# Performance work log

Hardware: AMD Instinct MI355X
Metric: run time of the kernel (lower is better)

## Reference

```python
import jax, jax.numpy as jnp
import numpy as np
from jax import lax

N, CIN, COUT, K = 16, 3, 16, 3
D = H = W = 64

def setup_inputs() -> dict:
    key = jax.random.key(0)
    k1, k2, k3 = jax.random.split(key, 3)
    x = jax.random.normal(k1, (N, CIN, D, H, W), dtype=jnp.float32)
    # torch Conv3d default init scale ~ 1/sqrt(fan_in); plain normals are fine for a baseline
    fan_in = CIN * K * K * K
    weight = jax.random.normal(k2, (COUT, CIN, K, K, K), dtype=jnp.float32) / np.sqrt(fan_in)
    bias = jax.random.normal(k3, (COUT,), dtype=jnp.float32) * 0.01
    return {"x": x, "weight": weight, "bias": bias}

def reference(x, weight, bias):
    # Conv3d, stride 1, no padding (NCDHW / OIDHW)
    y = lax.conv_general_dilated(
        x, weight,
        window_strides=(1, 1, 1),
        padding="VALID",
        dimension_numbers=("NCDHW", "OIDHW", "NCDHW"),
    )
    y = y + bias[None, :, None, None, None]          # [N, C, D', H', W']
    m = jnp.min(y, axis=2)                            # min over D -> [N, C, H', W']
    return jax.nn.softmax(m, axis=1)                  # softmax over channels
```

## Files before the change

kernel.cpp:

```cpp
#include <hip/hip_runtime.h>
#include <math.h>


#define CH 8

__global__ __launch_bounds__(1024)
__attribute__((amdgpu_waves_per_eu(8)))
void conv3d_min_softmax(
    const float* __restrict__ x,
    const float* __restrict__ wgt,
    const float* __restrict__ bias,
    float* __restrict__ out)
{
    const int tid = threadIdx.x;
    const int wv  = __builtin_amdgcn_readfirstlane(tid >> 6);
    const int l   = tid & 63;
    const int r0  = l >> 4;
    const int cg  = l & 15;
    const int wc  = cg * 2;
    const int n   = blockIdx.z;
    const int h0  = blockIdx.y * 4;
    const int w0  = blockIdx.x * 32;

    __shared__ __align__(16) float sx[2][5184];
    __shared__ float sm[128 * 17];

    const float bv = bias[wv];

    int goff[2];
#pragma unroll
    for (int k = 0; k < 2; ++k) {
        int F = tid + 1024 * k;
        if (F > 1295) F = 1295;
        int ci  = F / 432;
        int rem = F - ci * 432;
        int dd  = rem / 54;
        int rr  = rem - dd * 54;
        int rw  = rr / 9;
        int g   = rr - rw * 9;
        int gh  = h0 + rw;  if (gh > 63) gh = 63;
        int gw  = w0 + g * 4; if (gw > 60) gw = 60;
        goff[k] = (((ci * 64 + dd) * 64 + gh) * 64 + gw) * 4;
    }
    const char* xb = (const char*)(x + (size_t)n * 3 * 64 * 64 * 64);

    float Aacc[10][2];
#pragma unroll
    for (int j = 0; j < 10; ++j) { Aacc[j][0] = 0.f; Aacc[j][1] = 0.f; }
    float mv[2] = {1e30f, 1e30f};

    {
        char* lb = (char*)&sx[0][0];
        __builtin_amdgcn_global_load_lds(
            (const void*)(xb + goff[0]), (void*)(lb + tid * 16), 16, 0, 0);
        if (tid < 272)
            __builtin_amdgcn_global_load_lds(
                (const void*)(xb + goff[1]),
                (void*)(lb + (1024 + tid) * 16), 16, 0, 0);
    }

    for (int c = 0; c < 64 / CH; ++c) {
        __syncthreads();

        if (c < 7) {
            const char* xc = xb + (size_t)(c + 1) * (CH * 64 * 64 * 4);
            char* lb = (char*)&sx[(c + 1) & 1][0];
            __builtin_amdgcn_global_load_lds(
                (const void*)(xc + goff[0]), (void*)(lb + tid * 16),
                16, 0, 0);
            if (tid < 272)
                __builtin_amdgcn_global_load_lds(
                    (const void*)(xc + goff[1]),
                    (void*)(lb + (1024 + tid) * 16), 16, 0, 0);
        }

        const float* S = sx[c & 1];

#pragma unroll 1
        for (int ci = 0; ci < 3; ++ci) {
            float wsc[27];
            {
                const float* wp_ = wgt + (wv * 3 + ci) * 27;
#pragma unroll
                for (int i = 0; i < 27; ++i) wsc[i] = wp_[i];
            }
            const float* Sci = S + ci * (CH * 6 * 36) + r0 * 36 + wc;
#pragma unroll
            for (int dd = 0; dd < CH; ++dd) {
#pragma unroll
                for (int kh = 0; kh < 3; ++kh) {
                    const float2 a = *(const float2*)&Sci[(dd * 6 + kh) * 36];
                    const float2 b =
                        *(const float2*)&Sci[(dd * 6 + kh) * 36 + 2];
                    const float row[4] = {a.x, a.y, b.x, b.y};
#pragma unroll
                    for (int kw = 0; kw < 3; ++kw) {
                        const float wk0 = wsc[0  + kh * 3 + kw];
                        const float wk1 = wsc[9  + kh * 3 + kw];
                        const float wk2 = wsc[18 + kh * 3 + kw];
#pragma unroll
                        for (int p = 0; p < 2; ++p) {
                            const float xv = row[kw + p];
                            Aacc[dd + 2][p] = fmaf(xv, wk0, Aacc[dd + 2][p]);
                            Aacc[dd + 1][p] = fmaf(xv, wk1, Aacc[dd + 1][p]);
                            Aacc[dd + 0][p] = fmaf(xv, wk2, Aacc[dd + 0][p]);
                        }
                    }
                }
            }
        }

        const bool full = (c > 0);
#pragma unroll
        for (int j = 0; j < 8; ++j) {
            if (j >= 2 || full) {
                mv[0] = fminf(mv[0], Aacc[j][0]);
                mv[1] = fminf(mv[1], Aacc[j][1]);
            }
        }
#pragma unroll
        for (int p = 0; p < 2; ++p) {
            Aacc[0][p] = Aacc[8][p];
            Aacc[1][p] = Aacc[9][p];
        }
#pragma unroll
        for (int j = 2; j < 10; ++j) { Aacc[j][0] = 0.f; Aacc[j][1] = 0.f; }
    }

    const int px0 = r0 * 32 + wc;
    sm[px0 * 17 + wv]       = mv[0] + bv;
    sm[(px0 + 1) * 17 + wv] = mv[1] + bv;
    __syncthreads();

    const int hp = h0 + r0;
#pragma unroll
    for (int pp = 0; pp < 2; ++pp) {
        const int px = px0 + pp;
        float mx = -1e30f;
#pragma unroll
        for (int j = 0; j < 16; ++j) mx = fmaxf(mx, sm[px * 17 + j]);
        float sum = 0.f;
#pragma unroll
        for (int j = 0; j < 16; ++j) sum += __expf(sm[px * 17 + j] - mx);
        const int wp = w0 + wc + pp;
        if (hp < 62 && wp < 62) {
            const float e = __expf(sm[px * 17 + wv] - mx);
            out[(((size_t)n * 16 + wv) * 62 + hp) * 62 + wp] = e / sum;
        }
    }
}

extern "C" void kernel_launch(void* const* d_in, const int* in_sizes, int n_in,
                              void* d_out, int out_size, void* d_ws, size_t ws_size,
                              hipStream_t stream) {
    const float* x    = (const float*)d_in[0];
    const float* wgt  = (const float*)d_in[1];
    const float* bias = (const float*)d_in[2];
    float* out        = (float*)d_out;
    dim3 grid(2, 16, 16);
    dim3 block(1024);
    hipLaunchKernelGGL(conv3d_min_softmax, grid, block, 0, stream,
                       x, wgt, bias, out);
}
```

Before: 219.6 us.

## Enlarge per-thread tile to 4 outputs and block tile to 8 rows

Each thread now computes 4 adjacent W outputs instead of 2, and each block covers 8 H rows instead of 4, so the grid shrinks to 256 blocks. This reuses each LDS row load across more FMAs and lowers the halo overhead relative to the tile, cutting LDS traffic and redundant global loads. It roughly doubles accumulator registers, and the waves_per_eu(8) hint is dropped to allow that. The risks are lower occupancy and fewer blocks than needed to fill all CUs.

```diff
diff --git a/kernel.cpp b/kernel.cpp
--- a/kernel.cpp
+++ b/kernel.cpp
@@ -5,7 +5,6 @@
 #define CH 8
 
 __global__ __launch_bounds__(1024)
-__attribute__((amdgpu_waves_per_eu(8)))
 void conv3d_min_softmax(
     const float* __restrict__ x,
     const float* __restrict__ wgt,
@@ -15,27 +14,27 @@
     const int tid = threadIdx.x;
     const int wv  = __builtin_amdgcn_readfirstlane(tid >> 6);
     const int l   = tid & 63;
-    const int r0  = l >> 4;
-    const int cg  = l & 15;
-    const int wc  = cg * 2;
+    const int r0  = l >> 3;
+    const int cg  = l & 7;
+    const int wc  = cg * 4;
     const int n   = blockIdx.z;
-    const int h0  = blockIdx.y * 4;
+    const int h0  = blockIdx.y * 8;
     const int w0  = blockIdx.x * 32;
 
-    __shared__ __align__(16) float sx[2][5184];
-    __shared__ float sm[128 * 17];
+    __shared__ __align__(16) float sx[2][8640];
+    __shared__ float sm[256 * 17];
 
     const float bv = bias[wv];
 
-    int goff[2];
+    int goff[3];
 #pragma unroll
-    for (int k = 0; k < 2; ++k) {
+    for (int k = 0; k < 3; ++k) {
         int F = tid + 1024 * k;
-        if (F > 1295) F = 1295;
-        int ci  = F / 432;
-        int rem = F - ci * 432;
-        int dd  = rem / 54;
-        int rr  = rem - dd * 54;
+        if (F > 2159) F = 2159;
+        int ci  = F / 720;
+        int rem = F - ci * 720;
+        int dd  = rem / 90;
+        int rr  = rem - dd * 90;
         int rw  = rr / 9;
         int g   = rr - rw * 9;
         int gh  = h0 + rw;  if (gh > 63) gh = 63;
@@ -44,19 +43,24 @@
     }
     const char* xb = (const char*)(x + (size_t)n * 3 * 64 * 64 * 64);
 
-    float Aacc[10][2];
+    float Aacc[10][4];
 #pragma unroll
-    for (int j = 0; j < 10; ++j) { Aacc[j][0] = 0.f; Aacc[j][1] = 0.f; }
-    float mv[2] = {1e30f, 1e30f};
+    for (int j = 0; j < 10; ++j)
+#pragma unroll
+        for (int p = 0; p < 4; ++p) Aacc[j][p] = 0.f;
+    float mv[4] = {1e30f, 1e30f, 1e30f, 1e30f};
 
     {
         char* lb = (char*)&sx[0][0];
         __builtin_amdgcn_global_load_lds(
             (const void*)(xb + goff[0]), (void*)(lb + tid * 16), 16, 0, 0);
-        if (tid < 272)
+        __builtin_amdgcn_global_load_lds(
+            (const void*)(xb + goff[1]),
+            (void*)(lb + (1024 + tid) * 16), 16, 0, 0);
+        if (tid < 112)
             __builtin_amdgcn_global_load_lds(
-                (const void*)(xb + goff[1]),
-                (void*)(lb + (1024 + tid) * 16), 16, 0, 0);
+                (const void*)(xb + goff[2]),
+                (void*)(lb + (2048 + tid) * 16), 16, 0, 0);
     }
 
     for (int c = 0; c < 64 / CH; ++c) {
@@ -68,10 +72,13 @@
             __builtin_amdgcn_global_load_lds(
                 (const void*)(xc + goff[0]), (void*)(lb + tid * 16),
                 16, 0, 0);
-            if (tid < 272)
+            __builtin_amdgcn_global_load_lds(
+                (const void*)(xc + goff[1]),
+                (void*)(lb + (1024 + tid) * 16), 16, 0, 0);
+            if (tid < 112)
                 __builtin_amdgcn_global_load_lds(
-                    (const void*)(xc + goff[1]),
-                    (void*)(lb + (1024 + tid) * 16), 16, 0, 0);
+                    (const void*)(xc + goff[2]),
+                    (void*)(lb + (2048 + tid) * 16), 16, 0, 0);
         }
 
         const float* S = sx[c & 1];
@@ -84,22 +91,22 @@
 #pragma unroll
                 for (int i = 0; i < 27; ++i) wsc[i] = wp_[i];
             }
-            const float* Sci = S + ci * (CH * 6 * 36) + r0 * 36 + wc;
+            const float* Sci = S + ci * (CH * 10 * 36) + r0 * 36 + wc;
 #pragma unroll
             for (int dd = 0; dd < CH; ++dd) {
 #pragma unroll
                 for (int kh = 0; kh < 3; ++kh) {
-                    const float2 a = *(const float2*)&Sci[(dd * 6 + kh) * 36];
+                    const float4 a = *(const float4*)&Sci[(dd * 10 + kh) * 36];
                     const float2 b =
-                        *(const float2*)&Sci[(dd * 6 + kh) * 36 + 2];
-                    const float row[4] = {a.x, a.y, b.x, b.y};
+                        *(const float2*)&Sci[(dd * 10 + kh) * 36 + 4];
+                    const float row[6] = {a.x, a.y, a.z, a.w, b.x, b.y};
 #pragma unroll
                     for (int kw = 0; kw < 3; ++kw) {
                         const float wk0 = wsc[0  + kh * 3 + kw];
                         const float wk1 = wsc[9  + kh * 3 + kw];
                         const float wk2 = wsc[18 + kh * 3 + kw];
 #pragma unroll
-                        for (int p = 0; p < 2; ++p) {
+                        for (int p = 0; p < 4; ++p) {
                             const float xv = row[kw + p];
                             Aacc[dd + 2][p] = fmaf(xv, wk0, Aacc[dd + 2][p]);
                             Aacc[dd + 1][p] = fmaf(xv, wk1, Aacc[dd + 1][p]);
@@ -114,27 +121,31 @@
 #pragma unroll
         for (int j = 0; j < 8; ++j) {
             if (j >= 2 || full) {
-                mv[0] = fminf(mv[0], Aacc[j][0]);
-                mv[1] = fminf(mv[1], Aacc[j][1]);
+#pragma unroll
+                for (int p = 0; p < 4; ++p)
+                    mv[p] = fminf(mv[p], Aacc[j][p]);
             }
         }
 #pragma unroll
-        for (int p = 0; p < 2; ++p) {
+        for (int p = 0; p < 4; ++p) {
             Aacc[0][p] = Aacc[8][p];
             Aacc[1][p] = Aacc[9][p];
         }
 #pragma unroll
-        for (int j = 2; j < 10; ++j) { Aacc[j][0] = 0.f; Aacc[j][1] = 0.f; }
+        for (int j = 2; j < 10; ++j)
+#pragma unroll
+            for (int p = 0; p < 4; ++p) Aacc[j][p] = 0.f;
     }
 
     const int px0 = r0 * 32 + wc;
-    sm[px0 * 17 + wv]       = mv[0] + bv;
-    sm[(px0 + 1) * 17 + wv] = mv[1] + bv;
+#pragma unroll
+    for (int pp = 0; pp < 4; ++pp)
+        sm[(px0 + pp) * 17 + wv] = mv[pp] + bv;
     __syncthreads();
 
     const int hp = h0 + r0;
 #pragma unroll
-    for (int pp = 0; pp < 2; ++pp) {
+    for (int pp = 0; pp < 4; ++pp) {
         const int px = px0 + pp;
         float mx = -1e30f;
 #pragma unroll
@@ -157,7 +168,7 @@
     const float* wgt  = (const float*)d_in[1];
     const float* bias = (const float*)d_in[2];
     float* out        = (float*)d_out;
-    dim3 grid(2, 16, 16);
+    dim3 grid(2, 8, 16);
     dim3 block(1024);
     hipLaunchKernelGGL(conv3d_min_softmax, grid, block, 0, stream,
                        x, wgt, bias, out);
```

New measurement: 269.7 us. +22.8%, slower.
